# Kernel optimization log

Measured on AMD Instinct MI355X. Metric: run time of the kernel, lower is better.

Reference implementation:

```python
import jax, jax.numpy as jnp
import numpy as np

N_NODES = 25000
N_EDGES = 400000
CHANNELS = 32
EDGE_FEAT_DIM = 8
HIDDEN = 64
NUM_IRREPS = 4  # messages irreps = 2x0e + 2x1o -> 4 irreps, dim 8
AVG_NUM_NEIGHBORS = 16.0


def _mlp(x, W0, W1, W2, W3):
    # e3nn MultiLayerPerceptron: dense layers with 1/sqrt(fan_in) forward
    # normalization, silu on hidden layers, no output activation.
    for W in (W0, W1, W2):
        x = jax.nn.silu(x @ (W / jnp.sqrt(jnp.float32(W.shape[0]))))
    return x @ (W3 / jnp.sqrt(jnp.float32(W3.shape[0])))


def setup_inputs() -> dict:
    key = jax.random.key(0)
    ks = jax.random.split(key, 9)
    node_feats = jax.random.normal(ks[0], (N_NODES, CHANNELS, 4), jnp.float32)
    edge_attrs = jax.random.normal(ks[1], (N_EDGES, 4), jnp.float32)
    edge_feats = jax.random.normal(ks[2], (N_EDGES, EDGE_FEAT_DIM), jnp.float32)
    senders = jax.random.randint(ks[3], (N_EDGES,), 0, N_NODES)
    receivers = jax.random.randint(ks[4], (N_EDGES,), 0, N_NODES)
    W0 = jax.random.normal(ks[5], (EDGE_FEAT_DIM, HIDDEN), jnp.float32)
    W1 = jax.random.normal(ks[6], (HIDDEN, HIDDEN), jnp.float32)
    W2 = jax.random.normal(ks[7], (HIDDEN, HIDDEN), jnp.float32)
    W3 = jax.random.normal(ks[8], (HIDDEN, CHANNELS * NUM_IRREPS), jnp.float32)
    return {"node_feats": node_feats, "edge_attrs": edge_attrs,
            "edge_feats": edge_feats, "senders": senders, "receivers": receivers,
            "W0": W0, "W1": W1, "W2": W2, "W3": W3}


def reference(node_feats, edge_attrs, edge_feats, senders, receivers, W0, W1, W2, W3):
    # Gather sender node features: [E, C, 4] with irreps 0e (dim1) + 1o (dim3)
    x = node_feats[senders]
    s, v = x[..., 0], x[..., 1:4]            # [E,C], [E,C,3]
    a_s = edge_attrs[:, 0]                   # Y_0: [E]
    a_v = edge_attrs[:, 1:4]                 # Y_1: [E,3]

    # CG tensor product filtered to 0e + 1o (e3nn normalization: sqrt(2l3+1)*w3j)
    m0a = s * a_s[:, None]                                   # 0e x 0e -> 0e  [E,C]
    m0b = jnp.einsum('ecd,ed->ec', v, a_v) / jnp.sqrt(3.0)   # 1o x 1o -> 0e  [E,C]
    m1a = s[..., None] * a_v[:, None, :]                     # 0e x 1o -> 1o  [E,C,3]
    m1b = v * a_s[:, None, None]                             # 1o x 0e -> 1o  [E,C,3]

    # Edge MLP gate: [E, C*num_irreps] -> mul_to_axis -> [E, C, num_irreps]
    mix = _mlp(edge_feats, W0, W1, W2, W3).reshape(N_EDGES, CHANNELS, NUM_IRREPS)

    # Elementwise tensor product with 4x0e scalars: per-irrep gating
    out_s = jnp.stack([m0a * mix[..., 0], m0b * mix[..., 1]], axis=-1)          # [E,C,2]
    out_v = jnp.concatenate([m1a * mix[..., 2:3], m1b * mix[..., 3:4]], axis=-1)  # [E,C,6]
    messages = jnp.concatenate([out_s, out_v], axis=-1)                          # [E,C,8]

    # Scatter-add into receivers, then normalize by sqrt(avg_num_neighbors)
    agg = jax.ops.segment_sum(messages, receivers, num_segments=N_NODES)
    return agg / jnp.sqrt(AVG_NUM_NEIGHBORS)
```

## Files before the change

### kernel.cpp

```cpp
#include <hip/hip_runtime.h>
#include <hip/hip_fp16.h>

#define NE 400000
#define NN 25000
#define MAXDEG 56
#define LDS_STRIDE 65

typedef __attribute__((ext_vector_type(8))) _Float16 half8;
typedef __attribute__((ext_vector_type(4))) _Float16 half4;
typedef __attribute__((ext_vector_type(4))) float f32x4;

#define WS_MIX_OFF   0ull
#define WS_SLOTS_OFF 102400000ull
#define WS_CNT_OFF   108000000ull
#define WS_WBUF_OFF  108100000ull
#define WS_NEED      108136864ull

#define WB_L0 0
#define WB_L1 2048
#define WB_L2 6144
#define WB_L3 10240

__device__ __forceinline__ float fast_silu(float x) {
    float e = __expf(-x);
    return x * __builtin_amdgcn_rcpf(1.0f + e);
}

__global__ __launch_bounds__(64) void prep_weights(
    const float* __restrict__ W0, const float* __restrict__ W1,
    const float* __restrict__ W2, const float* __restrict__ W3,
    _Float16* __restrict__ wbuf, int* __restrict__ cnt)
{
    const int f    = blockIdx.x;
    const int lane = threadIdx.x;

    for (int i = f * 64 + lane; i < NN; i += 36 * 64) cnt[i] = 0;

    const int n    = lane & 15;
    const int quad = lane >> 4;

    const float* W; int K, N, kt, nt, fl, base; float scale;
    if (f < 4)       { W = W0; K = 8;  N = 64;  fl = f;      kt = 0;       nt = fl;     scale = 0.35355339059327373f; base = WB_L0; }
    else if (f < 12) { W = W1; K = 64; N = 64;  fl = f - 4;  kt = fl >> 2; nt = fl & 3; scale = 0.125f;   base = WB_L1; }
    else if (f < 20) { W = W2; K = 64; N = 64;  fl = f - 12; kt = fl >> 2; nt = fl & 3; scale = 0.125f;   base = WB_L2; }
    else             { W = W3; K = 64; N = 128; fl = f - 20; kt = fl >> 3; nt = fl & 7; scale = 0.03125f; base = WB_L3; }

    _Float16 v[8];
    #pragma unroll
    for (int j = 0; j < 8; ++j) {
        const int k = kt * 32 + quad * 8 + j;
        const float val = (k < K) ? W[k * N + nt * 16 + n] * scale : 0.0f;
        v[j] = (_Float16)val;
    }
    *(half8*)(wbuf + base + fl * 512 + lane * 8) = *(const half8*)v;
}

#define HS 72
__global__ __launch_bounds__(128, 4) void mlp_build_kernel(
    const float*    __restrict__ edge_feats,
    const int*      __restrict__ receivers,
    const _Float16* __restrict__ wbuf,
    int*            __restrict__ cnt,
    int*            __restrict__ slots,
    _Float16*       __restrict__ mix16)
{
    __shared__ _Float16 H[2 * 4 * 16 * HS];
    const int tid  = threadIdx.x;
    const int wave = tid >> 6;
    const int lane = tid & 63;
    const int col  = lane & 15;
    const int quad = lane >> 4;

    {
        const int e = blockIdx.x * 128 + tid;
        const int r = receivers[e];
        const int s = atomicAdd(&cnt[r], 1);
        if (s < MAXDEG) slots[r * MAXDEG + s] = e;
    }

    const int e0 = (blockIdx.x * 2 + wave) * 64;
    _Float16* HW = &H[wave * 4 * 16 * HS];
    const half8* wb = (const half8*)wbuf;
    const f32x4 zero4 = {0.f, 0.f, 0.f, 0.f};

    half8 b0[4];
    #pragma unroll
    for (int t = 0; t < 4; ++t) {
        half8 z = {0, 0, 0, 0, 0, 0, 0, 0};
        b0[t] = z;
    }
    if (quad == 0) {
        #pragma unroll
        for (int t = 0; t < 4; ++t) {
            const float4* p = (const float4*)(edge_feats + (size_t)(e0 + t * 16 + col) * 8);
            const float4 x = p[0], y = p[1];
            b0[t][0] = (_Float16)x.x; b0[t][1] = (_Float16)x.y; b0[t][2] = (_Float16)x.z; b0[t][3] = (_Float16)x.w;
            b0[t][4] = (_Float16)y.x; b0[t][5] = (_Float16)y.y; b0[t][6] = (_Float16)y.z; b0[t][7] = (_Float16)y.w;
        }
    }

    #pragma unroll
    for (int nt = 0; nt < 4; ++nt) {
        const half8 w = wb[(WB_L0 / 512 + nt) * 64 + lane];
        f32x4 a[4];
        #pragma unroll
        for (int t = 0; t < 4; ++t)
            a[t] = __builtin_amdgcn_mfma_f32_16x16x32_f16(w, b0[t], zero4, 0, 0, 0);
        #pragma unroll
        for (int t = 0; t < 4; ++t) {
            half4 h;
            #pragma unroll
            for (int r = 0; r < 4; ++r) h[r] = (_Float16)fast_silu(a[t][r]);
            *(half4*)&HW[t * 16 * HS + col * HS + nt * 16 + quad * 4] = h;
        }
    }

    #pragma unroll
    for (int layer = 0; layer < 2; ++layer) {
        const int wbase = (layer == 0 ? WB_L1 : WB_L2) / 512;
        half8 blo[4], bhi[4];
        #pragma unroll
        for (int t = 0; t < 4; ++t) {
            blo[t] = *(const half8*)&HW[t * 16 * HS + col * HS + 0  + quad * 8];
            bhi[t] = *(const half8*)&HW[t * 16 * HS + col * HS + 32 + quad * 8];
        }
        #pragma unroll
        for (int nt = 0; nt < 4; ++nt) {
            const half8 wlo = wb[(wbase + 0 + nt) * 64 + lane];
            const half8 whi = wb[(wbase + 4 + nt) * 64 + lane];
            f32x4 a[4];
            #pragma unroll
            for (int t = 0; t < 4; ++t) {
                a[t] = __builtin_amdgcn_mfma_f32_16x16x32_f16(wlo, blo[t], zero4, 0, 0, 0);
                a[t] = __builtin_amdgcn_mfma_f32_16x16x32_f16(whi, bhi[t], a[t], 0, 0, 0);
            }
            #pragma unroll
            for (int t = 0; t < 4; ++t) {
                half4 h;
                #pragma unroll
                for (int r = 0; r < 4; ++r) h[r] = (_Float16)fast_silu(a[t][r]);
                *(half4*)&HW[t * 16 * HS + col * HS + nt * 16 + quad * 4] = h;
            }
        }
    }

    {
        half8 blo[4], bhi[4];
        #pragma unroll
        for (int t = 0; t < 4; ++t) {
            blo[t] = *(const half8*)&HW[t * 16 * HS + col * HS + 0  + quad * 8];
            bhi[t] = *(const half8*)&HW[t * 16 * HS + col * HS + 32 + quad * 8];
        }
        _Float16* mrow0 = mix16 + (size_t)(e0 + 0 * 16 + col) * 128;
        _Float16* mrow1 = mix16 + (size_t)(e0 + 1 * 16 + col) * 128;
        _Float16* mrow2 = mix16 + (size_t)(e0 + 2 * 16 + col) * 128;
        _Float16* mrow3 = mix16 + (size_t)(e0 + 3 * 16 + col) * 128;
        _Float16* mrow[4] = {mrow0, mrow1, mrow2, mrow3};
        #pragma unroll
        for (int nt = 0; nt < 8; ++nt) {
            const half8 wlo = wb[(WB_L3 / 512 + 0 + nt) * 64 + lane];
            const half8 whi = wb[(WB_L3 / 512 + 8 + nt) * 64 + lane];
            #pragma unroll
            for (int t = 0; t < 4; ++t) {
                f32x4 a = __builtin_amdgcn_mfma_f32_16x16x32_f16(wlo, blo[t], zero4, 0, 0, 0);
                a = __builtin_amdgcn_mfma_f32_16x16x32_f16(whi, bhi[t], a, 0, 0, 0);
                half4 h;
                #pragma unroll
                for (int r = 0; r < 4; ++r) h[r] = (_Float16)a[r];
                *(half4*)&mrow[t][nt * 16 + quad * 4] = h;
            }
        }
    }
}

__global__ __launch_bounds__(64) void gather_kernel(
    const float*    __restrict__ node_feats,
    const float*    __restrict__ edge_attrs,
    const int*      __restrict__ senders,
    const _Float16* __restrict__ mix16,
    const int*      __restrict__ cnt,
    const int*      __restrict__ slots,
    float*          __restrict__ out)
{
    const int n    = blockIdx.x;
    const int lane = threadIdx.x;
    const int g    = lane >> 4;
    const int s    = lane & 15;
    const int c0   = 2 * s;
    const float inv_sqrt3 = 0.5773502691896258f;

    int d = cnt[n];
    if (d > MAXDEG) d = MAXDEG;
    const int* sl = slots + n * MAXDEG;

    const int li    = (lane < MAXDEG) ? lane : (MAXDEG - 1);
    int eid_l       = sl[li];
    eid_l           = (lane < d) ? eid_l : 0;
    const int snd_l = senders[eid_l];

    float acc[16];
    #pragma unroll
    for (int j = 0; j < 16; ++j) acc[j] = 0.0f;

    #pragma unroll 2
    for (int base = 0; base < d; base += 4) {
        const int  ei  = base + g;
        const bool act = (ei < d);
        const int  eid = __shfl(eid_l, ei, 64);
        const int  snd = __shfl(snd_l, ei, 64);
        const float4 a4v = ((const float4*)edge_attrs)[eid];
        const half8 m8 = *(const half8*)(mix16 + (size_t)eid * 128 + c0 * 4);
        const float4 xA = ((const float4*)(node_feats + (size_t)snd * 128))[c0];
        const float4 xB = ((const float4*)(node_feats + (size_t)snd * 128))[c0 + 1];

        const float z = act ? 1.0f : 0.0f;
        const float as = a4v.x, av0 = a4v.y, av1 = a4v.z, av2 = a4v.w;

        {
            const float m0 = z * (float)m8[0], m1 = z * (float)m8[1];
            const float m2 = z * (float)m8[2], m3 = z * (float)m8[3];
            const float sc = xA.x, v0 = xA.y, v1 = xA.z, v2 = xA.w;
            acc[0] = fmaf(sc * as, m0, acc[0]);
            const float dv = v0 * av0 + v1 * av1 + v2 * av2;
            acc[1] = fmaf(dv * inv_sqrt3, m1, acc[1]);
            acc[2] = fmaf(sc * av0, m2, acc[2]);
            acc[3] = fmaf(sc * av1, m2, acc[3]);
            acc[4] = fmaf(sc * av2, m2, acc[4]);
            acc[5] = fmaf(v0 * as, m3, acc[5]);
            acc[6] = fmaf(v1 * as, m3, acc[6]);
            acc[7] = fmaf(v2 * as, m3, acc[7]);
        }
        {
            const float m0 = z * (float)m8[4], m1 = z * (float)m8[5];
            const float m2 = z * (float)m8[6], m3 = z * (float)m8[7];
            const float sc = xB.x, v0 = xB.y, v1 = xB.z, v2 = xB.w;
            acc[8]  = fmaf(sc * as, m0, acc[8]);
            const float dv = v0 * av0 + v1 * av1 + v2 * av2;
            acc[9]  = fmaf(dv * inv_sqrt3, m1, acc[9]);
            acc[10] = fmaf(sc * av0, m2, acc[10]);
            acc[11] = fmaf(sc * av1, m2, acc[11]);
            acc[12] = fmaf(sc * av2, m2, acc[12]);
            acc[13] = fmaf(v0 * as, m3, acc[13]);
            acc[14] = fmaf(v1 * as, m3, acc[14]);
            acc[15] = fmaf(v2 * as, m3, acc[15]);
        }
    }

    #pragma unroll
    for (int j = 0; j < 16; ++j) {
        acc[j] += __shfl_xor(acc[j], 16, 64);
        acc[j] += __shfl_xor(acc[j], 32, 64);
    }

    if (g == 0) {
        float4* op = (float4*)(out + (size_t)n * 256 + s * 16);
        float4 r0; r0.x = acc[0];  r0.y = acc[1];  r0.z = acc[2];  r0.w = acc[3];
        float4 r1; r1.x = acc[4];  r1.y = acc[5];  r1.z = acc[6];  r1.w = acc[7];
        float4 r2; r2.x = acc[8];  r2.y = acc[9];  r2.z = acc[10]; r2.w = acc[11];
        float4 r3; r3.x = acc[12]; r3.y = acc[13]; r3.z = acc[14]; r3.w = acc[15];
        op[0] = r0; op[1] = r1; op[2] = r2; op[3] = r3;
    }
}

__global__ __launch_bounds__(128) void edge_mp_kernel(
    const float* __restrict__ node_feats, const float* __restrict__ edge_attrs,
    const float* __restrict__ edge_feats, const int* __restrict__ senders,
    const int* __restrict__ receivers, const float* __restrict__ W0,
    const float* __restrict__ W1, const float* __restrict__ W2,
    const float* __restrict__ W3, float* __restrict__ out)
{
    __shared__ float hbuf[128 * LDS_STRIDE];
    const int tid = threadIdx.x;
    const int e   = blockIdx.x * 128 + tid;
    if (e >= NE) return;
    float* hl = &hbuf[tid * LDS_STRIDE];

    float4 ef0 = ((const float4*)edge_feats)[e * 2 + 0];
    float4 ef1 = ((const float4*)edge_feats)[e * 2 + 1];
    float ef[8] = {ef0.x, ef0.y, ef0.z, ef0.w, ef1.x, ef1.y, ef1.z, ef1.w};
    float acc[64];
    #pragma unroll
    for (int i = 0; i < 64; ++i) acc[i] = 0.0f;
    #pragma unroll
    for (int j = 0; j < 8; ++j) {
        const float xj = ef[j];
        const float* wrow = W0 + j * 64;
        #pragma unroll
        for (int i = 0; i < 64; ++i) acc[i] = fmaf(xj, wrow[i], acc[i]);
    }
    {
        const float s0 = 0.35355339059327373f;
        #pragma unroll
        for (int i = 0; i < 64; ++i) hl[i] = fast_silu(acc[i] * s0);
    }
    #pragma unroll
    for (int i = 0; i < 64; ++i) acc[i] = 0.0f;
    #pragma unroll 4
    for (int j = 0; j < 64; ++j) {
        const float xj = hl[j];
        const float* wrow = W1 + j * 64;
        #pragma unroll
        for (int i = 0; i < 64; ++i) acc[i] = fmaf(xj, wrow[i], acc[i]);
    }
    #pragma unroll
    for (int i = 0; i < 64; ++i) hl[i] = fast_silu(acc[i] * 0.125f);
    #pragma unroll
    for (int i = 0; i < 64; ++i) acc[i] = 0.0f;
    #pragma unroll 4
    for (int j = 0; j < 64; ++j) {
        const float xj = hl[j];
        const float* wrow = W2 + j * 64;
        #pragma unroll
        for (int i = 0; i < 64; ++i) acc[i] = fmaf(xj, wrow[i], acc[i]);
    }
    float h2[64];
    #pragma unroll
    for (int i = 0; i < 64; ++i) h2[i] = fast_silu(acc[i] * 0.125f);

    const int snd = senders[e];
    const int rcv = receivers[e];
    const float4 a4 = ((const float4*)edge_attrs)[e];
    const float a_s = a4.x, av0 = a4.y, av1 = a4.z, av2 = a4.w;
    const float4* nf4 = (const float4*)(node_feats + (size_t)snd * 128);
    float* outp = out + (size_t)rcv * 256;
    const float mixscale = 0.03125f;
    const float inv_sqrt3 = 0.5773502691896258f;

    #pragma unroll 2
    for (int c = 0; c < 32; ++c) {
        float m0 = 0.0f, m1 = 0.0f, m2 = 0.0f, m3 = 0.0f;
        const float* wc = W3 + c * 4;
        #pragma unroll
        for (int j = 0; j < 64; ++j) {
            const float hj = h2[j];
            m0 = fmaf(hj, wc[j * 128 + 0], m0);
            m1 = fmaf(hj, wc[j * 128 + 1], m1);
            m2 = fmaf(hj, wc[j * 128 + 2], m2);
            m3 = fmaf(hj, wc[j * 128 + 3], m3);
        }
        m0 *= mixscale; m1 *= mixscale; m2 *= mixscale; m3 *= mixscale;
        const float4 x4 = nf4[c];
        const float s = x4.x, v0 = x4.y, v1 = x4.z, v2 = x4.w;
        float* op = outp + c * 8;
        atomicAdd(op + 0, s * a_s * m0);
        const float dotva = v0 * av0 + v1 * av1 + v2 * av2;
        atomicAdd(op + 1, dotva * inv_sqrt3 * m1);
        atomicAdd(op + 2, s * av0 * m2);
        atomicAdd(op + 3, s * av1 * m2);
        atomicAdd(op + 4, s * av2 * m2);
        atomicAdd(op + 5, v0 * a_s * m3);
        atomicAdd(op + 6, v1 * a_s * m3);
        atomicAdd(op + 7, v2 * a_s * m3);
    }
}

extern "C" void kernel_launch(void* const* d_in, const int* in_sizes, int n_in,
                              void* d_out, int out_size, void* d_ws, size_t ws_size,
                              hipStream_t stream) {
    const float* node_feats = (const float*)d_in[0];
    const float* edge_attrs = (const float*)d_in[1];
    const float* edge_feats = (const float*)d_in[2];
    const int*   senders    = (const int*)d_in[3];
    const int*   receivers  = (const int*)d_in[4];
    const float* W0 = (const float*)d_in[5];
    const float* W1 = (const float*)d_in[6];
    const float* W2 = (const float*)d_in[7];
    const float* W3 = (const float*)d_in[8];
    float* outp = (float*)d_out;

    if (ws_size >= WS_NEED) {
        char* w = (char*)d_ws;
        _Float16* mix16 = (_Float16*)(w + WS_MIX_OFF);
        int*      slots = (int*)(w + WS_SLOTS_OFF);
        int*      cnt   = (int*)(w + WS_CNT_OFF);
        _Float16* wbuf  = (_Float16*)(w + WS_WBUF_OFF);

        hipLaunchKernelGGL(prep_weights, dim3(36), dim3(64), 0, stream,
                           W0, W1, W2, W3, wbuf, cnt);
        hipLaunchKernelGGL(mlp_build_kernel, dim3(NE / 128), dim3(128), 0, stream,
                           edge_feats, receivers, wbuf, cnt, slots, mix16);
        hipLaunchKernelGGL(gather_kernel, dim3(NN), dim3(64), 0, stream,
                           node_feats, edge_attrs, senders, mix16, cnt, slots, outp);
    } else {
        hipMemsetAsync(d_out, 0, (size_t)out_size * sizeof(float), stream);
        hipLaunchKernelGGL(edge_mp_kernel, dim3((NE + 127) / 128), dim3(128), 0, stream,
                           node_feats, edge_attrs, edge_feats, senders, receivers,
                           W0, W1, W2, W3, outp);
    }
}
```

Measured before the change: 213.4 us.

## Fuse edge MLP into per-node gather, dropping the intermediate mix buffer

The edge MLP now runs inside the receiver-centric gather kernel, computed on 16-edge tiles per wave, so the last layer's MFMA output feeds the message accumulation directly. This removes the roughly 100 MB fp16 mix write and re-read through global memory. The CSR slot build moves into its own small kernel, and the MLP weights are staged in LDS for each block. In exchange, padded tiles waste MFMA work on nodes with few edges, blocks now use a large LDS footprint (weights plus H), and the per-node work is serial across tiles.

```diff
diff --git a/kernel.cpp b/kernel.cpp
--- a/kernel.cpp
+++ b/kernel.cpp
@@ -10,11 +10,10 @@
 typedef __attribute__((ext_vector_type(4))) _Float16 half4;
 typedef __attribute__((ext_vector_type(4))) float f32x4;
 
-#define WS_MIX_OFF   0ull
-#define WS_SLOTS_OFF 102400000ull
-#define WS_CNT_OFF   108000000ull
-#define WS_WBUF_OFF  108100000ull
-#define WS_NEED      108136864ull
+#define WS_SLOTS_OFF 0ull
+#define WS_CNT_OFF   5600000ull
+#define WS_WBUF_OFF  5700000ull
+#define WS_NEED      5736864ull
 
 #define WB_L0 0
 #define WB_L1 2048
@@ -55,138 +54,45 @@
     *(half8*)(wbuf + base + fl * 512 + lane * 8) = *(const half8*)v;
 }
 
-#define HS 72
-__global__ __launch_bounds__(128, 4) void mlp_build_kernel(
-    const float*    __restrict__ edge_feats,
-    const int*      __restrict__ receivers,
-    const _Float16* __restrict__ wbuf,
-    int*            __restrict__ cnt,
-    int*            __restrict__ slots,
-    _Float16*       __restrict__ mix16)
+__global__ __launch_bounds__(256) void csr_build(
+    const int* __restrict__ receivers, int* __restrict__ cnt, int* __restrict__ slots)
 {
-    __shared__ _Float16 H[2 * 4 * 16 * HS];
-    const int tid  = threadIdx.x;
-    const int wave = tid >> 6;
-    const int lane = tid & 63;
-    const int col  = lane & 15;
-    const int quad = lane >> 4;
-
-    {
-        const int e = blockIdx.x * 128 + tid;
+    const int e = blockIdx.x * 256 + threadIdx.x;
+    if (e < NE) {
         const int r = receivers[e];
         const int s = atomicAdd(&cnt[r], 1);
         if (s < MAXDEG) slots[r * MAXDEG + s] = e;
     }
-
-    const int e0 = (blockIdx.x * 2 + wave) * 64;
-    _Float16* HW = &H[wave * 4 * 16 * HS];
-    const half8* wb = (const half8*)wbuf;
-    const f32x4 zero4 = {0.f, 0.f, 0.f, 0.f};
-
-    half8 b0[4];
-    #pragma unroll
-    for (int t = 0; t < 4; ++t) {
-        half8 z = {0, 0, 0, 0, 0, 0, 0, 0};
-        b0[t] = z;
-    }
-    if (quad == 0) {
-        #pragma unroll
-        for (int t = 0; t < 4; ++t) {
-            const float4* p = (const float4*)(edge_feats + (size_t)(e0 + t * 16 + col) * 8);
-            const float4 x = p[0], y = p[1];
-            b0[t][0] = (_Float16)x.x; b0[t][1] = (_Float16)x.y; b0[t][2] = (_Float16)x.z; b0[t][3] = (_Float16)x.w;
-            b0[t][4] = (_Float16)y.x; b0[t][5] = (_Float16)y.y; b0[t][6] = (_Float16)y.z; b0[t][7] = (_Float16)y.w;
-        }
-    }
-
-    #pragma unroll
-    for (int nt = 0; nt < 4; ++nt) {
-        const half8 w = wb[(WB_L0 / 512 + nt) * 64 + lane];
-        f32x4 a[4];
-        #pragma unroll
-        for (int t = 0; t < 4; ++t)
-            a[t] = __builtin_amdgcn_mfma_f32_16x16x32_f16(w, b0[t], zero4, 0, 0, 0);
-        #pragma unroll
-        for (int t = 0; t < 4; ++t) {
-            half4 h;
-            #pragma unroll
-            for (int r = 0; r < 4; ++r) h[r] = (_Float16)fast_silu(a[t][r]);
-            *(half4*)&HW[t * 16 * HS + col * HS + nt * 16 + quad * 4] = h;
-        }
-    }
-
-    #pragma unroll
-    for (int layer = 0; layer < 2; ++layer) {
-        const int wbase = (layer == 0 ? WB_L1 : WB_L2) / 512;
-        half8 blo[4], bhi[4];
-        #pragma unroll
-        for (int t = 0; t < 4; ++t) {
-            blo[t] = *(const half8*)&HW[t * 16 * HS + col * HS + 0  + quad * 8];
-            bhi[t] = *(const half8*)&HW[t * 16 * HS + col * HS + 32 + quad * 8];
-        }
-        #pragma unroll
-        for (int nt = 0; nt < 4; ++nt) {
-            const half8 wlo = wb[(wbase + 0 + nt) * 64 + lane];
-            const half8 whi = wb[(wbase + 4 + nt) * 64 + lane];
-            f32x4 a[4];
-            #pragma unroll
-            for (int t = 0; t < 4; ++t) {
-                a[t] = __builtin_amdgcn_mfma_f32_16x16x32_f16(wlo, blo[t], zero4, 0, 0, 0);
-                a[t] = __builtin_amdgcn_mfma_f32_16x16x32_f16(whi, bhi[t], a[t], 0, 0, 0);
-            }
-            #pragma unroll
-            for (int t = 0; t < 4; ++t) {
-                half4 h;
-                #pragma unroll
-                for (int r = 0; r < 4; ++r) h[r] = (_Float16)fast_silu(a[t][r]);
-                *(half4*)&HW[t * 16 * HS + col * HS + nt * 16 + quad * 4] = h;
-            }
-        }
-    }
-
-    {
-        half8 blo[4], bhi[4];
-        #pragma unroll
-        for (int t = 0; t < 4; ++t) {
-            blo[t] = *(const half8*)&HW[t * 16 * HS + col * HS + 0  + quad * 8];
-            bhi[t] = *(const half8*)&HW[t * 16 * HS + col * HS + 32 + quad * 8];
-        }
-        _Float16* mrow0 = mix16 + (size_t)(e0 + 0 * 16 + col) * 128;
-        _Float16* mrow1 = mix16 + (size_t)(e0 + 1 * 16 + col) * 128;
-        _Float16* mrow2 = mix16 + (size_t)(e0 + 2 * 16 + col) * 128;
-        _Float16* mrow3 = mix16 + (size_t)(e0 + 3 * 16 + col) * 128;
-        _Float16* mrow[4] = {mrow0, mrow1, mrow2, mrow3};
-        #pragma unroll
-        for (int nt = 0; nt < 8; ++nt) {
-            const half8 wlo = wb[(WB_L3 / 512 + 0 + nt) * 64 + lane];
-            const half8 whi = wb[(WB_L3 / 512 + 8 + nt) * 64 + lane];
-            #pragma unroll
-            for (int t = 0; t < 4; ++t) {
-                f32x4 a = __builtin_amdgcn_mfma_f32_16x16x32_f16(wlo, blo[t], zero4, 0, 0, 0);
-                a = __builtin_amdgcn_mfma_f32_16x16x32_f16(whi, bhi[t], a, 0, 0, 0);
-                half4 h;
-                #pragma unroll
-                for (int r = 0; r < 4; ++r) h[r] = (_Float16)a[r];
-                *(half4*)&mrow[t][nt * 16 + quad * 4] = h;
-            }
-        }
-    }
-}
-
-__global__ __launch_bounds__(64) void gather_kernel(
+}
+
+#define HS 72
+__global__ __launch_bounds__(256) void fused_mp_kernel(
     const float*    __restrict__ node_feats,
     const float*    __restrict__ edge_attrs,
+    const float*    __restrict__ edge_feats,
     const int*      __restrict__ senders,
-    const _Float16* __restrict__ mix16,
+    const _Float16* __restrict__ wbuf,
     const int*      __restrict__ cnt,
     const int*      __restrict__ slots,
     float*          __restrict__ out)
 {
-    const int n    = blockIdx.x;
-    const int lane = threadIdx.x;
-    const int g    = lane >> 4;
-    const int s    = lane & 15;
-    const int c0   = 2 * s;
+    __shared__ _Float16 WL[18432];
+    __shared__ _Float16 H[4 * 16 * HS];
+
+    const int tid = threadIdx.x;
+    {
+        const half8* src = (const half8*)wbuf;
+        half8*       dst = (half8*)WL;
+        #pragma unroll
+        for (int i = 0; i < 9; ++i) dst[i * 256 + tid] = src[i * 256 + tid];
+    }
+    __syncthreads();
+
+    const int wave = tid >> 6;
+    const int lane = tid & 63;
+    const int c    = lane & 15;
+    const int q    = lane >> 4;
+    const int n    = blockIdx.x * 4 + wave;
     const float inv_sqrt3 = 0.5773502691896258f;
 
     int d = cnt[n];
@@ -198,67 +104,120 @@
     eid_l           = (lane < d) ? eid_l : 0;
     const int snd_l = senders[eid_l];
 
-    float acc[16];
-    #pragma unroll
-    for (int j = 0; j < 16; ++j) acc[j] = 0.0f;
-
-    #pragma unroll 2
-    for (int base = 0; base < d; base += 4) {
-        const int  ei  = base + g;
-        const bool act = (ei < d);
-        const int  eid = __shfl(eid_l, ei, 64);
-        const int  snd = __shfl(snd_l, ei, 64);
-        const float4 a4v = ((const float4*)edge_attrs)[eid];
-        const half8 m8 = *(const half8*)(mix16 + (size_t)eid * 128 + c0 * 4);
-        const float4 xA = ((const float4*)(node_feats + (size_t)snd * 128))[c0];
-        const float4 xB = ((const float4*)(node_feats + (size_t)snd * 128))[c0 + 1];
-
-        const float z = act ? 1.0f : 0.0f;
-        const float as = a4v.x, av0 = a4v.y, av1 = a4v.z, av2 = a4v.w;
+    float acc[8][8];
+    #pragma unroll
+    for (int nt = 0; nt < 8; ++nt)
+        #pragma unroll
+        for (int j = 0; j < 8; ++j) acc[nt][j] = 0.0f;
+
+    _Float16* HW = &H[wave * 16 * HS];
+    const half8* wb = (const half8*)WL;
+    const f32x4 zero4 = {0.f, 0.f, 0.f, 0.f};
+
+    const int ntiles = (d + 15) >> 4;
+    for (int t = 0; t < ntiles; ++t) {
+        const int  slot = t * 16 + c;
+        const int  eid  = __shfl(eid_l, slot, 64);
+        const int  snd  = __shfl(snd_l, slot, 64);
+        const bool act  = (slot < d);
+
+        half8 b0 = {0, 0, 0, 0, 0, 0, 0, 0};
+        if (q == 0) {
+            const float4* p = (const float4*)(edge_feats + (size_t)eid * 8);
+            const float4 x = p[0], y = p[1];
+            b0[0] = (_Float16)x.x; b0[1] = (_Float16)x.y; b0[2] = (_Float16)x.z; b0[3] = (_Float16)x.w;
+            b0[4] = (_Float16)y.x; b0[5] = (_Float16)y.y; b0[6] = (_Float16)y.z; b0[7] = (_Float16)y.w;
+        }
+
+        #pragma unroll
+        for (int nt = 0; nt < 4; ++nt) {
+            const half8 w = wb[(WB_L0 / 512 + nt) * 64 + lane];
+            f32x4 a = __builtin_amdgcn_mfma_f32_16x16x32_f16(w, b0, zero4, 0, 0, 0);
+            half4 h;
+            #pragma unroll
+            for (int r = 0; r < 4; ++r) h[r] = (_Float16)fast_silu(a[r]);
+            *(half4*)&HW[c * HS + nt * 16 + q * 4] = h;
+        }
+
+        #pragma unroll
+        for (int layer = 0; layer < 2; ++layer) {
+            const int wbase = (layer == 0 ? WB_L1 : WB_L2) / 512;
+            const half8 blo = *(const half8*)&HW[c * HS + 0  + q * 8];
+            const half8 bhi = *(const half8*)&HW[c * HS + 32 + q * 8];
+            f32x4 a[4];
+            #pragma unroll
+            for (int nt = 0; nt < 4; ++nt) {
+                const half8 wlo = wb[(wbase + 0 + nt) * 64 + lane];
+                const half8 whi = wb[(wbase + 4 + nt) * 64 + lane];
+                a[nt] = __builtin_amdgcn_mfma_f32_16x16x32_f16(wlo, blo, zero4, 0, 0, 0);
+                a[nt] = __builtin_amdgcn_mfma_f32_16x16x32_f16(whi, bhi, a[nt], 0, 0, 0);
+            }
+            #pragma unroll
+            for (int nt = 0; nt < 4; ++nt) {
+                half4 h;
+                #pragma unroll
+                for (int r = 0; r < 4; ++r) h[r] = (_Float16)fast_silu(a[nt][r]);
+                *(half4*)&HW[c * HS + nt * 16 + q * 4] = h;
+            }
+        }
 
         {
-            const float m0 = z * (float)m8[0], m1 = z * (float)m8[1];
-            const float m2 = z * (float)m8[2], m3 = z * (float)m8[3];
-            const float sc = xA.x, v0 = xA.y, v1 = xA.z, v2 = xA.w;
-            acc[0] = fmaf(sc * as, m0, acc[0]);
-            const float dv = v0 * av0 + v1 * av1 + v2 * av2;
-            acc[1] = fmaf(dv * inv_sqrt3, m1, acc[1]);
-            acc[2] = fmaf(sc * av0, m2, acc[2]);
-            acc[3] = fmaf(sc * av1, m2, acc[3]);
-            acc[4] = fmaf(sc * av2, m2, acc[4]);
-            acc[5] = fmaf(v0 * as, m3, acc[5]);
-            acc[6] = fmaf(v1 * as, m3, acc[6]);
-            acc[7] = fmaf(v2 * as, m3, acc[7]);
-        }
-        {
-            const float m0 = z * (float)m8[4], m1 = z * (float)m8[5];
-            const float m2 = z * (float)m8[6], m3 = z * (float)m8[7];
-            const float sc = xB.x, v0 = xB.y, v1 = xB.z, v2 = xB.w;
-            acc[8]  = fmaf(sc * as, m0, acc[8]);
-            const float dv = v0 * av0 + v1 * av1 + v2 * av2;
-            acc[9]  = fmaf(dv * inv_sqrt3, m1, acc[9]);
-            acc[10] = fmaf(sc * av0, m2, acc[10]);
-            acc[11] = fmaf(sc * av1, m2, acc[11]);
-            acc[12] = fmaf(sc * av2, m2, acc[12]);
-            acc[13] = fmaf(v0 * as, m3, acc[13]);
-            acc[14] = fmaf(v1 * as, m3, acc[14]);
-            acc[15] = fmaf(v2 * as, m3, acc[15]);
-        }
-    }
-
-    #pragma unroll
-    for (int j = 0; j < 16; ++j) {
-        acc[j] += __shfl_xor(acc[j], 16, 64);
-        acc[j] += __shfl_xor(acc[j], 32, 64);
-    }
-
-    if (g == 0) {
-        float4* op = (float4*)(out + (size_t)n * 256 + s * 16);
-        float4 r0; r0.x = acc[0];  r0.y = acc[1];  r0.z = acc[2];  r0.w = acc[3];
-        float4 r1; r1.x = acc[4];  r1.y = acc[5];  r1.z = acc[6];  r1.w = acc[7];
-        float4 r2; r2.x = acc[8];  r2.y = acc[9];  r2.z = acc[10]; r2.w = acc[11];
-        float4 r3; r3.x = acc[12]; r3.y = acc[13]; r3.z = acc[14]; r3.w = acc[15];
-        op[0] = r0; op[1] = r1; op[2] = r2; op[3] = r3;
+            const half8 blo = *(const half8*)&HW[c * HS + 0  + q * 8];
+            const half8 bhi = *(const half8*)&HW[c * HS + 32 + q * 8];
+
+            const float4 a4 = ((const float4*)edge_attrs)[eid];
+            const float as = a4.x, av0 = a4.y, av1 = a4.z, av2 = a4.w;
+            const float z  = act ? 1.0f : 0.0f;
+
+            const float4* nfp = (const float4*)(node_feats + (size_t)snd * 128);
+            float4 nf[8];
+            #pragma unroll
+            for (int nt = 0; nt < 8; ++nt) nf[nt] = nfp[4 * nt + q];
+
+            #pragma unroll
+            for (int nt = 0; nt < 8; ++nt) {
+                const half8 wlo = wb[(WB_L3 / 512 + 0 + nt) * 64 + lane];
+                const half8 whi = wb[(WB_L3 / 512 + 8 + nt) * 64 + lane];
+                f32x4 a = __builtin_amdgcn_mfma_f32_16x16x32_f16(wlo, blo, zero4, 0, 0, 0);
+                a = __builtin_amdgcn_mfma_f32_16x16x32_f16(whi, bhi, a, 0, 0, 0);
+                const float m0 = z * a[0], m1 = z * a[1];
+                const float m2 = z * a[2], m3 = z * a[3];
+                const float sc = nf[nt].x, v0 = nf[nt].y, v1 = nf[nt].z, v2 = nf[nt].w;
+                acc[nt][0] = fmaf(sc * as, m0, acc[nt][0]);
+                const float dv = v0 * av0 + v1 * av1 + v2 * av2;
+                acc[nt][1] = fmaf(dv * inv_sqrt3, m1, acc[nt][1]);
+                acc[nt][2] = fmaf(sc * av0, m2, acc[nt][2]);
+                acc[nt][3] = fmaf(sc * av1, m2, acc[nt][3]);
+                acc[nt][4] = fmaf(sc * av2, m2, acc[nt][4]);
+                acc[nt][5] = fmaf(v0 * as, m3, acc[nt][5]);
+                acc[nt][6] = fmaf(v1 * as, m3, acc[nt][6]);
+                acc[nt][7] = fmaf(v2 * as, m3, acc[nt][7]);
+            }
+        }
+    }
+
+    #pragma unroll
+    for (int nt = 0; nt < 8; ++nt)
+        #pragma unroll
+        for (int j = 0; j < 8; ++j) {
+            float v = acc[nt][j];
+            v += __shfl_xor(v, 1, 64);
+            v += __shfl_xor(v, 2, 64);
+            v += __shfl_xor(v, 4, 64);
+            v += __shfl_xor(v, 8, 64);
+            acc[nt][j] = v;
+        }
+
+    if (c == 0) {
+        float* op = out + (size_t)n * 256 + q * 8;
+        #pragma unroll
+        for (int nt = 0; nt < 8; ++nt) {
+            float4 lo, hi;
+            lo.x = acc[nt][0]; lo.y = acc[nt][1]; lo.z = acc[nt][2]; lo.w = acc[nt][3];
+            hi.x = acc[nt][4]; hi.y = acc[nt][5]; hi.z = acc[nt][6]; hi.w = acc[nt][7];
+            ((float4*)(op + nt * 32))[0] = lo;
+            ((float4*)(op + nt * 32 + 4))[0] = hi;
+        }
     }
 }
 
@@ -370,17 +329,17 @@
 
     if (ws_size >= WS_NEED) {
         char* w = (char*)d_ws;
-        _Float16* mix16 = (_Float16*)(w + WS_MIX_OFF);
         int*      slots = (int*)(w + WS_SLOTS_OFF);
         int*      cnt   = (int*)(w + WS_CNT_OFF);
         _Float16* wbuf  = (_Float16*)(w + WS_WBUF_OFF);
 
         hipLaunchKernelGGL(prep_weights, dim3(36), dim3(64), 0, stream,
                            W0, W1, W2, W3, wbuf, cnt);
-        hipLaunchKernelGGL(mlp_build_kernel, dim3(NE / 128), dim3(128), 0, stream,
-                           edge_feats, receivers, wbuf, cnt, slots, mix16);
-        hipLaunchKernelGGL(gather_kernel, dim3(NN), dim3(64), 0, stream,
-                           node_feats, edge_attrs, senders, mix16, cnt, slots, outp);
+        hipLaunchKernelGGL(csr_build, dim3((NE + 255) / 256), dim3(256), 0, stream,
+                           receivers, cnt, slots);
+        hipLaunchKernelGGL(fused_mp_kernel, dim3(NN / 4), dim3(256), 0, stream,
+                           node_feats, edge_attrs, edge_feats, senders,
+                           wbuf, cnt, slots, outp);
     } else {
         hipMemsetAsync(d_out, 0, (size_t)out_size * sizeof(float), stream);
         hipLaunchKernelGGL(edge_mp_kernel, dim3((NE + 127) / 128), dim3(128), 0, stream,
```

Result: slower. 364.9 us (+71.0%).
